# Kernel tuning notes

Hardware: AMD Instinct MI355X
Metric: run time of the kernel (lower is better)

## Reference

```python
import jax, jax.numpy as jnp
import numpy as np

B, L, D, A = 64, 196, 2048, 1024  # batch, locations, hidden_size, att_hid_size


def setup_inputs() -> dict:
    key = jax.random.key(0)
    ks = jax.random.split(key, 8)
    scale = 0.02
    return {
        "att_features": jax.random.normal(ks[0], (B, L, D), dtype=jnp.float32),
        "h": jax.random.normal(ks[1], (B, D), dtype=jnp.float32),
        "W_att": jax.random.normal(ks[2], (D, A), dtype=jnp.float32) * scale,
        "b_att": jnp.zeros((A,), dtype=jnp.float32),
        "W_h": jax.random.normal(ks[3], (D, A), dtype=jnp.float32) * scale,
        "b_h": jnp.zeros((A,), dtype=jnp.float32),
        "w_alpha": jax.random.normal(ks[4], (A, 1), dtype=jnp.float32) * scale,
        "b_alpha": jnp.zeros((1,), dtype=jnp.float32),
    }


def reference(att_features, h, W_att, b_att, W_h, b_h, w_alpha, b_alpha):
    b = att_features.shape[0]
    d = att_features.shape[-1]
    locations = att_features.size // b // d
    af = att_features.reshape(b, locations, d)            # [B, L, D]
    p_att = af @ W_att + b_att                            # [B, L, A]
    p_h = (h @ W_h + b_h)[:, None, :]                     # [B, 1, A]
    scores = (jnp.tanh(p_att + p_h) @ w_alpha + b_alpha)[..., 0]  # [B, L]
    weights = jax.nn.softmax(scores, axis=1)              # [B, L]
    weighted = jnp.einsum('bl,bld->bd', weights, af)      # [B, D]
    return weighted, weights
```

## Files before the change

kernel.cpp:

```cpp
#include <hip/hip_runtime.h>


typedef unsigned short u16;
typedef u16 u16x8 __attribute__((ext_vector_type(8)));
typedef __bf16 bf16x8 __attribute__((ext_vector_type(8)));
typedef float f32x4 __attribute__((ext_vector_type(4)));

#define B_ 64
#define L_ 196
#define D_ 2048
#define A_ 1024
#define M_ (B_ * L_)

__device__ __forceinline__ u16 f2bf(float x) {
  unsigned u = __float_as_uint(x);
  unsigned r = (u + 0x7fffu + ((u >> 16) & 1u)) >> 16;
  return (u16)r;
}

__device__ __forceinline__ float tanh_fast(float x) {
  float e = __expf(2.0f * x);
  return 1.0f - 2.0f / (e + 1.0f);
}

__device__ __forceinline__ void gload_lds16(const void* g, void* l) {
  __builtin_amdgcn_global_load_lds(
      (const __attribute__((address_space(1))) void*)g,
      (__attribute__((address_space(3))) void*)l, 16, 0, 0);
}

__global__ __launch_bounds__(256) void prep_k(
    const float* __restrict__ af, u16* __restrict__ afb,
    const float* __restrict__ W, u16* __restrict__ WT,
    const float* __restrict__ h, const float* __restrict__ Wh,
    float* __restrict__ ph) {
  __shared__ float smem[2112];
  const int bid = blockIdx.x;
  const int t = threadIdx.x;
  if (bid < 256) {
    const int ag = bid & 3, bg = (bid >> 2) & 7, dc = bid >> 5;
    const int d0 = dc * 256;
    for (int i = t; i < 2048; i += 256)
      smem[i] = h[(size_t)(bg * 8 + (i >> 8)) * D_ + d0 + (i & 255)];
    __syncthreads();
    const int a = ag * 256 + t;
    float acc[8] = {};
#pragma unroll 8
    for (int d = 0; d < 256; ++d) {
      float wv = Wh[(size_t)(d0 + d) * A_ + a];
#pragma unroll
      for (int bb = 0; bb < 8; ++bb) acc[bb] += smem[bb * 256 + d] * wv;
    }
#pragma unroll
    for (int bb = 0; bb < 8; ++bb)
      atomicAdd(&ph[(size_t)(bg * 8 + bb) * A_ + a], acc[bb]);
  } else if (bid < 2304) {
    const int tb = bid - 256;
    const int n0 = (tb & 31) * 32, k0 = (tb >> 5) * 32;
    const int tx = t & 31, ty = t >> 5;
    float (*tt)[33] = (float (*)[33])smem;
#pragma unroll
    for (int i = 0; i < 4; ++i)
      tt[ty + i * 8][tx] = W[(size_t)(k0 + ty + i * 8) * A_ + n0 + tx];
    __syncthreads();
#pragma unroll
    for (int i = 0; i < 4; ++i)
      WT[(size_t)(n0 + ty + i * 8) * D_ + k0 + tx] = f2bf(tt[tx][ty + i * 8]);
  } else {
    const int cb = bid - 2304;
    const size_t n = (size_t)M_ * D_;
    for (size_t e = ((size_t)cb * 256 + t) * 8; e < n;
         e += (size_t)2048 * 256 * 8) {
      float4 v0 = *(const float4*)(af + e);
      float4 v1 = *(const float4*)(af + e + 4);
      u16x8 p;
      p[0] = f2bf(v0.x); p[1] = f2bf(v0.y); p[2] = f2bf(v0.z); p[3] = f2bf(v0.w);
      p[4] = f2bf(v1.x); p[5] = f2bf(v1.y); p[6] = f2bf(v1.z); p[7] = f2bf(v1.w);
      *(u16x8*)(afb + e) = p;
    }
  }
}

__global__ __launch_bounds__(512, 2) void gemm8_k(
    const u16* __restrict__ afb, const u16* __restrict__ WT,
    const float* __restrict__ ph, const float* __restrict__ batt,
    const float* __restrict__ bh, const float* __restrict__ walpha,
    float* __restrict__ scores4) {
  __shared__ __align__(16) u16 As[2][2][8192];
  __shared__ __align__(16) u16 Bs[2][2][8192];
  const int tid = threadIdx.x;
  const int lane = tid & 63;
  const int wid = tid >> 6;
  const int wr = wid >> 2;
  const int wc = wid & 3;
  const int wchalf = wc >> 1, wcl = wc & 1;
  const int fr = lane & 15, fq = lane >> 4;

  const int xcd = blockIdx.x & 7, idx = blockIdx.x >> 3;
  const int wg = (xcd < 4 ? xcd * 25 : 100 + (xcd - 4) * 24) + idx;
  const int m0 = (wg >> 2) * 256;
  const int n0 = (wg & 3) * 256;

  int rowc[2], colc[2];
#pragma unroll
  for (int r = 0; r < 2; ++r) {
    int c = r * 512 + tid;
    int s = c >> 6, cw = c & 63;
    rowc[r] = (s >> 1) * 16 + (cw >> 2);
    colc[r] = (s & 1) * 32 + ((((cw & 3) * 16) ^ (((cw >> 5) & 1) * 32)) >> 1);
  }
  const u16* srcA[2][2];
  const u16* srcB[2][2];
#pragma unroll
  for (int hh = 0; hh < 2; ++hh)
#pragma unroll
    for (int r = 0; r < 2; ++r) {
      srcA[hh][r] = afb + (size_t)(m0 + hh * 128 + rowc[r]) * D_ + colc[r];
      srcB[hh][r] = WT + (size_t)(n0 + hh * 128 + rowc[r]) * D_ + colc[r];
    }

  const int laneA = (lane & 15) * 64 + (((lane >> 4) * 16) ^ ((lane & 8) << 2));

  f32x4 acc[8][4] = {};
  u16x8 areg[4][2], breg[4][2];

#define STG_A(BUF, H, KT)                                                    \
  do {                                                                       \
    gload_lds16(srcA[H][0] + (size_t)(KT) * 64, &As[BUF][H][wid * 512]);     \
    gload_lds16(srcA[H][1] + (size_t)(KT) * 64, &As[BUF][H][4096 + wid * 512]); \
  } while (0)
#define STG_B(BUF, H, KT)                                                    \
  do {                                                                       \
    gload_lds16(srcB[H][0] + (size_t)(KT) * 64, &Bs[BUF][H][wid * 512]);     \
    gload_lds16(srcB[H][1] + (size_t)(KT) * 64, &Bs[BUF][H][4096 + wid * 512]); \
  } while (0)
#define LDA_HALF(BF, MH)                                                     \
  do {                                                                       \
    _Pragma("unroll") for (int q = 0; q < 4; ++q) {                          \
      areg[q][0] = *(const u16x8*)&As[BF][wr][((((MH)*4 + q) * 2 + 0) * 1024 + laneA) >> 1]; \
      areg[q][1] = *(const u16x8*)&As[BF][wr][((((MH)*4 + q) * 2 + 1) * 1024 + laneA) >> 1]; \
    }                                                                        \
  } while (0)
#define LDB_PAIR(BF, NQ)                                                     \
  do {                                                                       \
    _Pragma("unroll") for (int nn = 0; nn < 2; ++nn) {                       \
      breg[(NQ)*2 + nn][0] = *(const u16x8*)&Bs[BF][wchalf][(((wcl * 4 + (NQ)*2 + nn) * 2 + 0) * 1024 + laneA) >> 1]; \
      breg[(NQ)*2 + nn][1] = *(const u16x8*)&Bs[BF][wchalf][(((wcl * 4 + (NQ)*2 + nn) * 2 + 1) * 1024 + laneA) >> 1]; \
    }                                                                        \
  } while (0)
#define MM_QUAD(MH, NQ)                                                      \
  do {                                                                       \
    _Pragma("unroll") for (int q = 0; q < 4; ++q)                            \
    _Pragma("unroll") for (int nn = 0; nn < 2; ++nn)                         \
    _Pragma("unroll") for (int kh = 0; kh < 2; ++kh)                         \
      acc[(MH)*4 + q][(NQ)*2 + nn] = __builtin_amdgcn_mfma_f32_16x16x32_bf16( \
          __builtin_bit_cast(bf16x8, areg[q][kh]),                           \
          __builtin_bit_cast(bf16x8, breg[(NQ)*2 + nn][kh]),                 \
          acc[(MH)*4 + q][(NQ)*2 + nn], 0, 0, 0);                            \
  } while (0)
#define PH_PRE()                                                             \
  do {                                                                       \
    __builtin_amdgcn_s_barrier();                                            \
    asm volatile("s_waitcnt lgkmcnt(0)" ::: "memory");                       \
    __builtin_amdgcn_s_setprio(1);                                           \
  } while (0)
#define PH_POST()                                                            \
  do {                                                                       \
    __builtin_amdgcn_s_setprio(0);                                           \
    __builtin_amdgcn_s_barrier();                                            \
  } while (0)
#define KTILE(BF, T, MODE)                                                   \
  do {                                                                       \
    LDA_HALF(BF, 0); LDB_PAIR(BF, 0); LDB_PAIR(BF, 1);                       \
    if ((MODE) <= 1) STG_A((BF) ^ 1, 1, (T) + 1);                            \
    PH_PRE(); MM_QUAD(0, 0); MM_QUAD(0, 1); PH_POST();                       \
    LDA_HALF(BF, 1);                                                         \
    if ((MODE) == 0) { STG_B(BF, 0, (T) + 2); STG_B(BF, 1, (T) + 2);         \
                       STG_A(BF, 0, (T) + 2); }                              \
    PH_PRE(); MM_QUAD(1, 0); MM_QUAD(1, 1);                                  \
    __builtin_amdgcn_s_setprio(0);                                           \
    if ((MODE) == 0) asm volatile("s_waitcnt vmcnt(6)" ::: "memory");        \
    if ((MODE) == 1) asm volatile("s_waitcnt vmcnt(0)" ::: "memory");        \
    if ((MODE) <= 1) __builtin_amdgcn_s_barrier();                           \
  } while (0)

  STG_B(0, 0, 0); STG_B(0, 1, 0); STG_A(0, 0, 0); STG_A(0, 1, 0);
  STG_B(1, 0, 1); STG_B(1, 1, 1); STG_A(1, 0, 1);
  asm volatile("s_waitcnt vmcnt(6)" ::: "memory");
  __builtin_amdgcn_s_barrier();

#pragma unroll 1
  for (int it = 0; it < 15; ++it) {
    const int t = it * 2;
    KTILE(0, t, 0);
    KTILE(1, t + 1, 0);
  }
  KTILE(0, 30, 1);
  KTILE(1, 31, 2);

  const int gnb = n0 + wc * 64 + fr;
  float wa[4], bsv[4], p0[4], p1[4], p2[4];
  const int b0 = m0 / L_;
  const int s1 = (b0 + 1) * L_, s2 = (b0 + 2) * L_;
  const int b1 = (b0 + 1 > 63) ? 63 : b0 + 1;
  const int b2 = (b0 + 2 > 63) ? 63 : b0 + 2;
#pragma unroll
  for (int ni = 0; ni < 4; ++ni) {
    const int gn = gnb + ni * 16;
    wa[ni] = walpha[gn];
    bsv[ni] = batt[gn] + bh[gn];
    p0[ni] = ph[(size_t)b0 * A_ + gn];
    p1[ni] = ph[(size_t)b1 * A_ + gn];
    p2[ni] = ph[(size_t)b2 * A_ + gn];
  }
  float (*redp)[128][4] = (float (*)[128][4])As;
#pragma unroll
  for (int mi = 0; mi < 8; ++mi) {
#pragma unroll
    for (int rr = 0; rr < 4; ++rr) {
      const int lr = mi * 16 + fq * 4 + rr;
      const int gm = m0 + wr * 128 + lr;
      float sp = 0.f;
#pragma unroll
      for (int ni = 0; ni < 4; ++ni) {
        const float pv = (gm >= s2) ? p2[ni] : ((gm >= s1) ? p1[ni] : p0[ni]);
        const float p = acc[mi][ni][rr] + pv + bsv[ni];
        sp += tanh_fast(p) * wa[ni];
      }
      sp += __shfl_xor(sp, 1);
      sp += __shfl_xor(sp, 2);
      sp += __shfl_xor(sp, 4);
      sp += __shfl_xor(sp, 8);
      if (fr == 0) redp[wr][lr][wc] = sp;
    }
  }
  __syncthreads();
  if (tid < 256) {
    f32x4 v = ((const f32x4*)redp)[tid];
    scores4[(size_t)(n0 >> 8) * M_ + m0 + tid] = v[0] + v[1] + v[2] + v[3];
  }
}

__global__ __launch_bounds__(256) void wsum_sm_k(const u16* __restrict__ afb,
                                                 const float* __restrict__ s4,
                                                 float* __restrict__ out) {
  __shared__ float wl[256];
  __shared__ float part[256][8];
  __shared__ float red[4];
  const int b = blockIdx.y;
  const int t = threadIdx.x;

  float s = -1e30f;
  if (t < L_) {
    const int i = b * L_ + t;
    s = s4[i] + s4[M_ + i] + s4[2 * M_ + i] + s4[3 * M_ + i];
  }
  float m = s;
#pragma unroll
  for (int o = 32; o; o >>= 1) m = fmaxf(m, __shfl_xor(m, o));
  if ((t & 63) == 0) red[t >> 6] = m;
  __syncthreads();
  m = fmaxf(fmaxf(red[0], red[1]), fmaxf(red[2], red[3]));
  float e = (t < L_) ? __expf(s - m) : 0.f;
  float sum = e;
#pragma unroll
  for (int o = 32; o; o >>= 1) sum += __shfl_xor(sum, o);
  __syncthreads();
  if ((t & 63) == 0) red[t >> 6] = sum;
  __syncthreads();
  sum = red[0] + red[1] + red[2] + red[3];
  const float w = e / sum;
  wl[t] = w;
  if (t < L_ && blockIdx.x == 0) out[(size_t)B_ * D_ + b * L_ + t] = w;
  __syncthreads();

  const int lq = t >> 6;
  const int dl = t & 63;
  const int d8 = blockIdx.x * 64 + dl;
  float acc[8] = {};
  for (int l = lq * 49; l < lq * 49 + 49; ++l) {
    u16x8 v = *(const u16x8*)(afb + (size_t)(b * L_ + l) * D_ + d8 * 8);
    float ww = wl[l];
#pragma unroll
    for (int j = 0; j < 8; ++j)
      acc[j] += ww * __uint_as_float((unsigned)v[j] << 16);
  }
#pragma unroll
  for (int j = 0; j < 8; ++j) part[t][j] = acc[j];
  __syncthreads();
  if (t < 64) {
    float4 o0, o1;
    o0.x = part[dl][0] + part[64 + dl][0] + part[128 + dl][0] + part[192 + dl][0];
    o0.y = part[dl][1] + part[64 + dl][1] + part[128 + dl][1] + part[192 + dl][1];
    o0.z = part[dl][2] + part[64 + dl][2] + part[128 + dl][2] + part[192 + dl][2];
    o0.w = part[dl][3] + part[64 + dl][3] + part[128 + dl][3] + part[192 + dl][3];
    o1.x = part[dl][4] + part[64 + dl][4] + part[128 + dl][4] + part[192 + dl][4];
    o1.y = part[dl][5] + part[64 + dl][5] + part[128 + dl][5] + part[192 + dl][5];
    o1.z = part[dl][6] + part[64 + dl][6] + part[128 + dl][6] + part[192 + dl][6];
    o1.w = part[dl][7] + part[64 + dl][7] + part[128 + dl][7] + part[192 + dl][7];
    *(float4*)(out + (size_t)b * D_ + d8 * 8) = o0;
    *(float4*)(out + (size_t)b * D_ + d8 * 8 + 4) = o1;
  }
}

extern "C" void kernel_launch(void* const* d_in, const int* in_sizes, int n_in,
                              void* d_out, int out_size, void* d_ws, size_t ws_size,
                              hipStream_t stream) {
  const float* af    = (const float*)d_in[0];
  const float* h     = (const float*)d_in[1];
  const float* W_att = (const float*)d_in[2];
  const float* b_att = (const float*)d_in[3];
  const float* W_h   = (const float*)d_in[4];
  const float* b_h   = (const float*)d_in[5];
  const float* w_al  = (const float*)d_in[6];
  float* out = (float*)d_out;
  char* ws = (char*)d_ws;

  u16* afb       = (u16*)ws;
  u16* WT        = (u16*)(ws + 0x3200000);
  float* ph      = (float*)(ws + 0x3600000);
  float* scores4 = (float*)(ws + 0x3640000);

  hipMemsetAsync(ph, 0, 256u << 10, stream);
  prep_k<<<4352, 256, 0, stream>>>(af, afb, W_att, WT, h, W_h, ph);
  gemm8_k<<<196, 512, 0, stream>>>(afb, WT, ph, b_att, b_h, w_al, scores4);
  wsum_sm_k<<<dim3(4, 64), 256, 0, stream>>>(afb, scores4, out);
}
```

Measured before the change: 119.2 us.

## Load B operand directly from global into registers, dropping LDS staging

The weight (B) tile is no longer staged through shared memory. Each wave loads its own 64 columns straight from global memory into double-buffered registers, while A keeps its LDS double buffer. The hand-tuned pipeline with split phases and explicit vmcnt waits is replaced by a simpler single-barrier-per-tile loop. This halves LDS usage and cuts LDS traffic, but B is now fetched redundantly by the two wave rows, uses more registers, and loses the fine-grained scheduling of the old pipeline.

```diff
diff --git a/kernel.cpp b/kernel.cpp
--- a/kernel.cpp
+++ b/kernel.cpp
@@ -87,13 +87,11 @@
     const float* __restrict__ bh, const float* __restrict__ walpha,
     float* __restrict__ scores4) {
   __shared__ __align__(16) u16 As[2][2][8192];
-  __shared__ __align__(16) u16 Bs[2][2][8192];
   const int tid = threadIdx.x;
   const int lane = tid & 63;
   const int wid = tid >> 6;
   const int wr = wid >> 2;
   const int wc = wid & 3;
-  const int wchalf = wc >> 1, wcl = wc & 1;
   const int fr = lane & 15, fq = lane >> 4;
 
   const int xcd = blockIdx.x & 7, idx = blockIdx.x >> 3;
@@ -110,93 +108,66 @@
     colc[r] = (s & 1) * 32 + ((((cw & 3) * 16) ^ (((cw >> 5) & 1) * 32)) >> 1);
   }
   const u16* srcA[2][2];
-  const u16* srcB[2][2];
 #pragma unroll
   for (int hh = 0; hh < 2; ++hh)
 #pragma unroll
-    for (int r = 0; r < 2; ++r) {
+    for (int r = 0; r < 2; ++r)
       srcA[hh][r] = afb + (size_t)(m0 + hh * 128 + rowc[r]) * D_ + colc[r];
-      srcB[hh][r] = WT + (size_t)(n0 + hh * 128 + rowc[r]) * D_ + colc[r];
-    }
+
+  const u16* bsrc = WT + (size_t)(n0 + wc * 64 + fr) * D_;
 
   const int laneA = (lane & 15) * 64 + (((lane >> 4) * 16) ^ ((lane & 8) << 2));
 
   f32x4 acc[8][4] = {};
-  u16x8 areg[4][2], breg[4][2];
+  u16x8 areg[4];
+  u16x8 bA[4][2], bB[4][2];
 
 #define STG_A(BUF, H, KT)                                                    \
   do {                                                                       \
     gload_lds16(srcA[H][0] + (size_t)(KT) * 64, &As[BUF][H][wid * 512]);     \
     gload_lds16(srcA[H][1] + (size_t)(KT) * 64, &As[BUF][H][4096 + wid * 512]); \
   } while (0)
-#define STG_B(BUF, H, KT)                                                    \
+#define BLOAD(BREG, T)                                                       \
   do {                                                                       \
-    gload_lds16(srcB[H][0] + (size_t)(KT) * 64, &Bs[BUF][H][wid * 512]);     \
-    gload_lds16(srcB[H][1] + (size_t)(KT) * 64, &Bs[BUF][H][4096 + wid * 512]); \
+    _Pragma("unroll") for (int n_ = 0; n_ < 4; ++n_)                         \
+    _Pragma("unroll") for (int kh_ = 0; kh_ < 2; ++kh_)                      \
+      BREG[n_][kh_] = *(const u16x8*)(bsrc + (size_t)n_ * 16 * D_ +          \
+                                      (size_t)(T) * 64 + kh_ * 32 + fq * 8); \
   } while (0)
-#define LDA_HALF(BF, MH)                                                     \
+#define TILE(BF, BCUR, BNXT, T, LAST)                                        \
   do {                                                                       \
-    _Pragma("unroll") for (int q = 0; q < 4; ++q) {                          \
-      areg[q][0] = *(const u16x8*)&As[BF][wr][((((MH)*4 + q) * 2 + 0) * 1024 + laneA) >> 1]; \
-      areg[q][1] = *(const u16x8*)&As[BF][wr][((((MH)*4 + q) * 2 + 1) * 1024 + laneA) >> 1]; \
+    if (!(LAST)) {                                                           \
+      STG_A((BF) ^ 1, 0, (T) + 1);                                           \
+      STG_A((BF) ^ 1, 1, (T) + 1);                                           \
+      BLOAD(BNXT, (T) + 1);                                                  \
     }                                                                        \
+    _Pragma("unroll") for (int mh_ = 0; mh_ < 2; ++mh_)                      \
+    _Pragma("unroll") for (int kh_ = 0; kh_ < 2; ++kh_) {                    \
+      _Pragma("unroll") for (int q_ = 0; q_ < 4; ++q_)                       \
+        areg[q_] = *(const u16x8*)&As[BF][wr][                               \
+            (((mh_ * 4 + q_) * 2 + kh_) * 1024 + laneA) >> 1];               \
+      __builtin_amdgcn_s_setprio(1);                                         \
+      _Pragma("unroll") for (int q_ = 0; q_ < 4; ++q_)                       \
+      _Pragma("unroll") for (int n_ = 0; n_ < 4; ++n_)                       \
+        acc[mh_ * 4 + q_][n_] = __builtin_amdgcn_mfma_f32_16x16x32_bf16(     \
+            __builtin_bit_cast(bf16x8, areg[q_]),                            \
+            __builtin_bit_cast(bf16x8, BCUR[n_][kh_]),                       \
+            acc[mh_ * 4 + q_][n_], 0, 0, 0);                                 \
+      __builtin_amdgcn_s_setprio(0);                                         \
+    }                                                                        \
+    __syncthreads();                                                         \
   } while (0)
-#define LDB_PAIR(BF, NQ)                                                     \
-  do {                                                                       \
-    _Pragma("unroll") for (int nn = 0; nn < 2; ++nn) {                       \
-      breg[(NQ)*2 + nn][0] = *(const u16x8*)&Bs[BF][wchalf][(((wcl * 4 + (NQ)*2 + nn) * 2 + 0) * 1024 + laneA) >> 1]; \
-      breg[(NQ)*2 + nn][1] = *(const u16x8*)&Bs[BF][wchalf][(((wcl * 4 + (NQ)*2 + nn) * 2 + 1) * 1024 + laneA) >> 1]; \
-    }                                                                        \
-  } while (0)
-#define MM_QUAD(MH, NQ)                                                      \
-  do {                                                                       \
-    _Pragma("unroll") for (int q = 0; q < 4; ++q)                            \
-    _Pragma("unroll") for (int nn = 0; nn < 2; ++nn)                         \
-    _Pragma("unroll") for (int kh = 0; kh < 2; ++kh)                         \
-      acc[(MH)*4 + q][(NQ)*2 + nn] = __builtin_amdgcn_mfma_f32_16x16x32_bf16( \
-          __builtin_bit_cast(bf16x8, areg[q][kh]),                           \
-          __builtin_bit_cast(bf16x8, breg[(NQ)*2 + nn][kh]),                 \
-          acc[(MH)*4 + q][(NQ)*2 + nn], 0, 0, 0);                            \
-  } while (0)
-#define PH_PRE()                                                             \
-  do {                                                                       \
-    __builtin_amdgcn_s_barrier();                                            \
-    asm volatile("s_waitcnt lgkmcnt(0)" ::: "memory");                       \
-    __builtin_amdgcn_s_setprio(1);                                           \
-  } while (0)
-#define PH_POST()                                                            \
-  do {                                                                       \
-    __builtin_amdgcn_s_setprio(0);                                           \
-    __builtin_amdgcn_s_barrier();                                            \
-  } while (0)
-#define KTILE(BF, T, MODE)                                                   \
-  do {                                                                       \
-    LDA_HALF(BF, 0); LDB_PAIR(BF, 0); LDB_PAIR(BF, 1);                       \
-    if ((MODE) <= 1) STG_A((BF) ^ 1, 1, (T) + 1);                            \
-    PH_PRE(); MM_QUAD(0, 0); MM_QUAD(0, 1); PH_POST();                       \
-    LDA_HALF(BF, 1);                                                         \
-    if ((MODE) == 0) { STG_B(BF, 0, (T) + 2); STG_B(BF, 1, (T) + 2);         \
-                       STG_A(BF, 0, (T) + 2); }                              \
-    PH_PRE(); MM_QUAD(1, 0); MM_QUAD(1, 1);                                  \
-    __builtin_amdgcn_s_setprio(0);                                           \
-    if ((MODE) == 0) asm volatile("s_waitcnt vmcnt(6)" ::: "memory");        \
-    if ((MODE) == 1) asm volatile("s_waitcnt vmcnt(0)" ::: "memory");        \
-    if ((MODE) <= 1) __builtin_amdgcn_s_barrier();                           \
-  } while (0)
-
-  STG_B(0, 0, 0); STG_B(0, 1, 0); STG_A(0, 0, 0); STG_A(0, 1, 0);
-  STG_B(1, 0, 1); STG_B(1, 1, 1); STG_A(1, 0, 1);
-  asm volatile("s_waitcnt vmcnt(6)" ::: "memory");
-  __builtin_amdgcn_s_barrier();
+
+  STG_A(0, 0, 0);
+  STG_A(0, 1, 0);
+  BLOAD(bA, 0);
+  __syncthreads();
 
 #pragma unroll 1
-  for (int it = 0; it < 15; ++it) {
-    const int t = it * 2;
-    KTILE(0, t, 0);
-    KTILE(1, t + 1, 0);
-  }
-  KTILE(0, 30, 1);
-  KTILE(1, 31, 2);
+  for (int it = 0; it < 16; ++it) {
+    TILE(0, bA, bB, 2 * it, false);
+    TILE(1, bB, bA, 2 * it + 1, (2 * it + 1) == 31);
+  }
 
   const int gnb = n0 + wc * 64 + fr;
   float wa[4], bsv[4], p0[4], p1[4], p2[4];
```

After: 152.0 us. +27.6%, slower.

## Fuse fp32-to-bf16 conversion of activations into GEMM A-tile loading

Applied to the files above, without the earlier changes.

Drops the separate pass that converted the whole activation tensor to bf16 in a workspace. The GEMM now loads fp32 activations into registers, converts them, and writes them into LDS with the swizzled layout. The weighted-sum kernel also reads the fp32 activations directly with twice as many blocks. This removes a full write and re-read of a large bf16 copy, at the cost of reading fp32 (twice the bytes) for A inside the GEMM with register staging instead of direct-to-LDS loads, and a shallower pipeline (prefetch one tile ahead instead of two).

```diff
diff --git a/kernel.cpp b/kernel.cpp
--- a/kernel.cpp
+++ b/kernel.cpp
@@ -30,7 +30,6 @@
 }
 
 __global__ __launch_bounds__(256) void prep_k(
-    const float* __restrict__ af, u16* __restrict__ afb,
     const float* __restrict__ W, u16* __restrict__ WT,
     const float* __restrict__ h, const float* __restrict__ Wh,
     float* __restrict__ ph) {
@@ -54,7 +53,7 @@
 #pragma unroll
     for (int bb = 0; bb < 8; ++bb)
       atomicAdd(&ph[(size_t)(bg * 8 + bb) * A_ + a], acc[bb]);
-  } else if (bid < 2304) {
+  } else {
     const int tb = bid - 256;
     const int n0 = (tb & 31) * 32, k0 = (tb >> 5) * 32;
     const int tx = t & 31, ty = t >> 5;
@@ -66,23 +65,11 @@
 #pragma unroll
     for (int i = 0; i < 4; ++i)
       WT[(size_t)(n0 + ty + i * 8) * D_ + k0 + tx] = f2bf(tt[tx][ty + i * 8]);
-  } else {
-    const int cb = bid - 2304;
-    const size_t n = (size_t)M_ * D_;
-    for (size_t e = ((size_t)cb * 256 + t) * 8; e < n;
-         e += (size_t)2048 * 256 * 8) {
-      float4 v0 = *(const float4*)(af + e);
-      float4 v1 = *(const float4*)(af + e + 4);
-      u16x8 p;
-      p[0] = f2bf(v0.x); p[1] = f2bf(v0.y); p[2] = f2bf(v0.z); p[3] = f2bf(v0.w);
-      p[4] = f2bf(v1.x); p[5] = f2bf(v1.y); p[6] = f2bf(v1.z); p[7] = f2bf(v1.w);
-      *(u16x8*)(afb + e) = p;
-    }
   }
 }
 
 __global__ __launch_bounds__(512, 2) void gemm8_k(
-    const u16* __restrict__ afb, const u16* __restrict__ WT,
+    const float* __restrict__ af, const u16* __restrict__ WT,
     const float* __restrict__ ph, const float* __restrict__ batt,
     const float* __restrict__ bh, const float* __restrict__ walpha,
     float* __restrict__ scores4) {
@@ -101,6 +88,19 @@
   const int m0 = (wg >> 2) * 256;
   const int n0 = (wg & 3) * 256;
 
+  const float* aSrc[4];
+  int aHh[4], aLds[4];
+#pragma unroll
+  for (int r = 0; r < 4; ++r) {
+    const int c = r * 512 + tid;
+    const int hh = c >> 10, cl = c & 1023;
+    const int row = cl >> 3, cc = cl & 7;
+    aHh[r] = hh;
+    aSrc[r] = af + (size_t)(m0 + hh * 128 + row) * D_ + cc * 8;
+    aLds[r] = ((row >> 4) * 2 + (cc >> 2)) * 512 + (row & 15) * 32 +
+              (((cc & 3) * 8) ^ ((row & 8) << 1));
+  }
+
   int rowc[2], colc[2];
 #pragma unroll
   for (int r = 0; r < 2; ++r) {
@@ -109,27 +109,19 @@
     rowc[r] = (s >> 1) * 16 + (cw >> 2);
     colc[r] = (s & 1) * 32 + ((((cw & 3) * 16) ^ (((cw >> 5) & 1) * 32)) >> 1);
   }
-  const u16* srcA[2][2];
   const u16* srcB[2][2];
 #pragma unroll
   for (int hh = 0; hh < 2; ++hh)
 #pragma unroll
-    for (int r = 0; r < 2; ++r) {
-      srcA[hh][r] = afb + (size_t)(m0 + hh * 128 + rowc[r]) * D_ + colc[r];
+    for (int r = 0; r < 2; ++r)
       srcB[hh][r] = WT + (size_t)(n0 + hh * 128 + rowc[r]) * D_ + colc[r];
-    }
 
   const int laneA = (lane & 15) * 64 + (((lane >> 4) * 16) ^ ((lane & 8) << 2));
 
   f32x4 acc[8][4] = {};
   u16x8 areg[4][2], breg[4][2];
 
-#define STG_A(BUF, H, KT)                                                    \
-  do {                                                                       \
-    gload_lds16(srcA[H][0] + (size_t)(KT) * 64, &As[BUF][H][wid * 512]);     \
-    gload_lds16(srcA[H][1] + (size_t)(KT) * 64, &As[BUF][H][4096 + wid * 512]); \
-  } while (0)
-#define STG_B(BUF, H, KT)                                                    \
+#define STG_B2(BUF, H, KT)                                                   \
   do {                                                                       \
     gload_lds16(srcB[H][0] + (size_t)(KT) * 64, &Bs[BUF][H][wid * 512]);     \
     gload_lds16(srcB[H][1] + (size_t)(KT) * 64, &Bs[BUF][H][4096 + wid * 512]); \
@@ -158,45 +150,79 @@
           __builtin_bit_cast(bf16x8, breg[(NQ)*2 + nn][kh]),                 \
           acc[(MH)*4 + q][(NQ)*2 + nn], 0, 0, 0);                            \
   } while (0)
-#define PH_PRE()                                                             \
-  do {                                                                       \
+#define LGKM_BAR()                                                           \
+  do {                                                                       \
+    asm volatile("s_waitcnt lgkmcnt(0)" ::: "memory");                       \
     __builtin_amdgcn_s_barrier();                                            \
-    asm volatile("s_waitcnt lgkmcnt(0)" ::: "memory");                       \
+  } while (0)
+#define TILE(BF, T, MODE)                                                    \
+  do {                                                                       \
+    float4 a4[4][2];                                                         \
+    if ((MODE) == 0) {                                                       \
+      _Pragma("unroll") for (int r = 0; r < 4; ++r) {                        \
+        a4[r][0] = *(const float4*)(aSrc[r] + (size_t)((T) + 1) * 64);       \
+        a4[r][1] = *(const float4*)(aSrc[r] + (size_t)((T) + 1) * 64 + 4);   \
+      }                                                                      \
+      STG_B2((BF) ^ 1, 0, (T) + 1);                                         \
+      STG_B2((BF) ^ 1, 1, (T) + 1);                                         \
+    }                                                                        \
+    LDA_HALF(BF, 0); LDB_PAIR(BF, 0); LDB_PAIR(BF, 1);                       \
+    LGKM_BAR();                                                              \
     __builtin_amdgcn_s_setprio(1);                                           \
-  } while (0)
-#define PH_POST()                                                            \
-  do {                                                                       \
+    MM_QUAD(0, 0); MM_QUAD(0, 1);                                            \
     __builtin_amdgcn_s_setprio(0);                                           \
-    __builtin_amdgcn_s_barrier();                                            \
-  } while (0)
-#define KTILE(BF, T, MODE)                                                   \
-  do {                                                                       \
-    LDA_HALF(BF, 0); LDB_PAIR(BF, 0); LDB_PAIR(BF, 1);                       \
-    if ((MODE) <= 1) STG_A((BF) ^ 1, 1, (T) + 1);                            \
-    PH_PRE(); MM_QUAD(0, 0); MM_QUAD(0, 1); PH_POST();                       \
     LDA_HALF(BF, 1);                                                         \
-    if ((MODE) == 0) { STG_B(BF, 0, (T) + 2); STG_B(BF, 1, (T) + 2);         \
-                       STG_A(BF, 0, (T) + 2); }                              \
-    PH_PRE(); MM_QUAD(1, 0); MM_QUAD(1, 1);                                  \
+    if ((MODE) == 0) {                                                       \
+      _Pragma("unroll") for (int r = 0; r < 4; ++r) {                        \
+        u16x8 p;                                                             \
+        p[0] = f2bf(a4[r][0].x); p[1] = f2bf(a4[r][0].y);                    \
+        p[2] = f2bf(a4[r][0].z); p[3] = f2bf(a4[r][0].w);                    \
+        p[4] = f2bf(a4[r][1].x); p[5] = f2bf(a4[r][1].y);                    \
+        p[6] = f2bf(a4[r][1].z); p[7] = f2bf(a4[r][1].w);                    \
+        *(u16x8*)&As[(BF) ^ 1][aHh[r]][aLds[r]] = p;                         \
+      }                                                                      \
+    }                                                                        \
+    LGKM_BAR();                                                              \
+    __builtin_amdgcn_s_setprio(1);                                           \
+    MM_QUAD(1, 0); MM_QUAD(1, 1);                                            \
     __builtin_amdgcn_s_setprio(0);                                           \
-    if ((MODE) == 0) asm volatile("s_waitcnt vmcnt(6)" ::: "memory");        \
-    if ((MODE) == 1) asm volatile("s_waitcnt vmcnt(0)" ::: "memory");        \
-    if ((MODE) <= 1) __builtin_amdgcn_s_barrier();                           \
-  } while (0)
-
-  STG_B(0, 0, 0); STG_B(0, 1, 0); STG_A(0, 0, 0); STG_A(0, 1, 0);
-  STG_B(1, 0, 1); STG_B(1, 1, 1); STG_A(1, 0, 1);
-  asm volatile("s_waitcnt vmcnt(6)" ::: "memory");
-  __builtin_amdgcn_s_barrier();
+    if ((MODE) == 0) {                                                       \
+      asm volatile("s_waitcnt vmcnt(0)" ::: "memory");                       \
+      LGKM_BAR();                                                            \
+    }                                                                        \
+  } while (0)
+
+  {
+    float4 a4[4][2];
+#pragma unroll
+    for (int r = 0; r < 4; ++r) {
+      a4[r][0] = *(const float4*)(aSrc[r]);
+      a4[r][1] = *(const float4*)(aSrc[r] + 4);
+    }
+    STG_B2(0, 0, 0);
+    STG_B2(0, 1, 0);
+#pragma unroll
+    for (int r = 0; r < 4; ++r) {
+      u16x8 p;
+      p[0] = f2bf(a4[r][0].x); p[1] = f2bf(a4[r][0].y);
+      p[2] = f2bf(a4[r][0].z); p[3] = f2bf(a4[r][0].w);
+      p[4] = f2bf(a4[r][1].x); p[5] = f2bf(a4[r][1].y);
+      p[6] = f2bf(a4[r][1].z); p[7] = f2bf(a4[r][1].w);
+      *(u16x8*)&As[0][aHh[r]][aLds[r]] = p;
+    }
+    asm volatile("s_waitcnt vmcnt(0) lgkmcnt(0)" ::: "memory");
+    __builtin_amdgcn_s_barrier();
+  }
 
 #pragma unroll 1
-  for (int it = 0; it < 15; ++it) {
-    const int t = it * 2;
-    KTILE(0, t, 0);
-    KTILE(1, t + 1, 0);
-  }
-  KTILE(0, 30, 1);
-  KTILE(1, 31, 2);
+  for (int it = 0; it < 16; ++it) {
+    TILE(0, 2 * it, 0);
+    if (it < 15) {
+      TILE(1, 2 * it + 1, 0);
+    } else {
+      TILE(1, 31, 1);
+    }
+  }
 
   const int gnb = n0 + wc * 64 + fr;
   float wa[4], bsv[4], p0[4], p1[4], p2[4];
@@ -213,6 +239,7 @@
     p1[ni] = ph[(size_t)b1 * A_ + gn];
     p2[ni] = ph[(size_t)b2 * A_ + gn];
   }
+  __syncthreads();
   float (*redp)[128][4] = (float (*)[128][4])As;
 #pragma unroll
   for (int mi = 0; mi < 8; ++mi) {
@@ -241,11 +268,11 @@
   }
 }
 
-__global__ __launch_bounds__(256) void wsum_sm_k(const u16* __restrict__ afb,
+__global__ __launch_bounds__(256) void wsum_sm_k(const float* __restrict__ af,
                                                  const float* __restrict__ s4,
                                                  float* __restrict__ out) {
   __shared__ float wl[256];
-  __shared__ float part[256][8];
+  __shared__ f32x4 part[256];
   __shared__ float red[4];
   const int b = blockIdx.y;
   const int t = threadIdx.x;
@@ -276,30 +303,17 @@
 
   const int lq = t >> 6;
   const int dl = t & 63;
-  const int d8 = blockIdx.x * 64 + dl;
-  float acc[8] = {};
+  const int d4 = blockIdx.x * 64 + dl;
+  f32x4 acc = {0.f, 0.f, 0.f, 0.f};
   for (int l = lq * 49; l < lq * 49 + 49; ++l) {
-    u16x8 v = *(const u16x8*)(afb + (size_t)(b * L_ + l) * D_ + d8 * 8);
-    float ww = wl[l];
-#pragma unroll
-    for (int j = 0; j < 8; ++j)
-      acc[j] += ww * __uint_as_float((unsigned)v[j] << 16);
-  }
-#pragma unroll
-  for (int j = 0; j < 8; ++j) part[t][j] = acc[j];
+    f32x4 v = *(const f32x4*)(af + (size_t)(b * L_ + l) * D_ + d4 * 4);
+    acc += v * wl[l];
+  }
+  part[t] = acc;
   __syncthreads();
   if (t < 64) {
-    float4 o0, o1;
-    o0.x = part[dl][0] + part[64 + dl][0] + part[128 + dl][0] + part[192 + dl][0];
-    o0.y = part[dl][1] + part[64 + dl][1] + part[128 + dl][1] + part[192 + dl][1];
-    o0.z = part[dl][2] + part[64 + dl][2] + part[128 + dl][2] + part[192 + dl][2];
-    o0.w = part[dl][3] + part[64 + dl][3] + part[128 + dl][3] + part[192 + dl][3];
-    o1.x = part[dl][4] + part[64 + dl][4] + part[128 + dl][4] + part[192 + dl][4];
-    o1.y = part[dl][5] + part[64 + dl][5] + part[128 + dl][5] + part[192 + dl][5];
-    o1.z = part[dl][6] + part[64 + dl][6] + part[128 + dl][6] + part[192 + dl][6];
-    o1.w = part[dl][7] + part[64 + dl][7] + part[128 + dl][7] + part[192 + dl][7];
-    *(float4*)(out + (size_t)b * D_ + d8 * 8) = o0;
-    *(float4*)(out + (size_t)b * D_ + d8 * 8 + 4) = o1;
+    f32x4 tot = part[t] + part[64 + t] + part[128 + t] + part[192 + t];
+    *(f32x4*)(out + (size_t)b * D_ + d4 * 4) = tot;
   }
 }
 
@@ -316,13 +330,12 @@
   float* out = (float*)d_out;
   char* ws = (char*)d_ws;
 
-  u16* afb       = (u16*)ws;
-  u16* WT        = (u16*)(ws + 0x3200000);
-  float* ph      = (float*)(ws + 0x3600000);
-  float* scores4 = (float*)(ws + 0x3640000);
+  u16* WT        = (u16*)ws;
+  float* ph      = (float*)(ws + 0x400000);
+  float* scores4 = (float*)(ws + 0x440000);
 
   hipMemsetAsync(ph, 0, 256u << 10, stream);
-  prep_k<<<4352, 256, 0, stream>>>(af, afb, W_att, WT, h, W_h, ph);
-  gemm8_k<<<196, 512, 0, stream>>>(afb, WT, ph, b_att, b_h, w_al, scores4);
-  wsum_sm_k<<<dim3(4, 64), 256, 0, stream>>>(afb, scores4, out);
-}
+  prep_k<<<2304, 256, 0, stream>>>(W_att, WT, h, W_h, ph);
+  gemm8_k<<<196, 512, 0, stream>>>(af, WT, ph, b_att, b_h, w_al, scores4);
+  wsum_sm_k<<<dim3(8, 64), 256, 0, stream>>>(af, scores4, out);
+}
```

New measurement: 353.3 us. 2.96x slower.

## Shrink GEMM tile to 256x64 and launch 784 blocks for better CU occupancy

Applied to the files above, without the earlier changes.

Changes the fused GEMM+tanh+score kernel from 256x256 tiles over 196 blocks to 256x64 tiles over 784 blocks. Each wave now owns 32 rows and all 64 columns, so the cross-wave LDS reduction is dropped and every wave writes its partial scores directly. There are now 16 partial score planes, which the softmax kernel sums. The goal is to fill the 256 CUs, since 196 blocks left many idle. The cost is four times more loading of the A operand and lower arithmetic intensity per block.

```diff
diff --git a/kernel.cpp b/kernel.cpp
--- a/kernel.cpp
+++ b/kernel.cpp
@@ -81,25 +81,21 @@
   }
 }
 
-__global__ __launch_bounds__(512, 2) void gemm8_k(
+__global__ __launch_bounds__(512, 4) void gemm8_k(
     const u16* __restrict__ afb, const u16* __restrict__ WT,
     const float* __restrict__ ph, const float* __restrict__ batt,
     const float* __restrict__ bh, const float* __restrict__ walpha,
-    float* __restrict__ scores4) {
+    float* __restrict__ scores16) {
   __shared__ __align__(16) u16 As[2][2][8192];
-  __shared__ __align__(16) u16 Bs[2][2][8192];
+  __shared__ __align__(16) u16 Bs[2][4096];
   const int tid = threadIdx.x;
   const int lane = tid & 63;
   const int wid = tid >> 6;
-  const int wr = wid >> 2;
-  const int wc = wid & 3;
-  const int wchalf = wc >> 1, wcl = wc & 1;
   const int fr = lane & 15, fq = lane >> 4;
 
-  const int xcd = blockIdx.x & 7, idx = blockIdx.x >> 3;
-  const int wg = (xcd < 4 ? xcd * 25 : 100 + (xcd - 4) * 24) + idx;
-  const int m0 = (wg >> 2) * 256;
-  const int n0 = (wg & 3) * 256;
+  const int wg = (blockIdx.x & 7) * 98 + (blockIdx.x >> 3);
+  const int m0 = (wg >> 4) * 256;
+  const int n0 = (wg & 15) * 64;
 
   int rowc[2], colc[2];
 #pragma unroll
@@ -110,53 +106,45 @@
     colc[r] = (s & 1) * 32 + ((((cw & 3) * 16) ^ (((cw >> 5) & 1) * 32)) >> 1);
   }
   const u16* srcA[2][2];
-  const u16* srcB[2][2];
 #pragma unroll
   for (int hh = 0; hh < 2; ++hh)
 #pragma unroll
-    for (int r = 0; r < 2; ++r) {
+    for (int r = 0; r < 2; ++r)
       srcA[hh][r] = afb + (size_t)(m0 + hh * 128 + rowc[r]) * D_ + colc[r];
-      srcB[hh][r] = WT + (size_t)(n0 + hh * 128 + rowc[r]) * D_ + colc[r];
-    }
+  const u16* srcB = WT + (size_t)(n0 + rowc[0]) * D_ + colc[0];
 
   const int laneA = (lane & 15) * 64 + (((lane >> 4) * 16) ^ ((lane & 8) << 2));
-
-  f32x4 acc[8][4] = {};
-  u16x8 areg[4][2], breg[4][2];
+  const int ahh = wid >> 2;
+  const int arow2 = (wid & 3) * 2;
+
+  f32x4 acc[2][4] = {};
+  u16x8 areg[2][2], breg[4][2];
 
 #define STG_A(BUF, H, KT)                                                    \
   do {                                                                       \
     gload_lds16(srcA[H][0] + (size_t)(KT) * 64, &As[BUF][H][wid * 512]);     \
     gload_lds16(srcA[H][1] + (size_t)(KT) * 64, &As[BUF][H][4096 + wid * 512]); \
   } while (0)
-#define STG_B(BUF, H, KT)                                                    \
-  do {                                                                       \
-    gload_lds16(srcB[H][0] + (size_t)(KT) * 64, &Bs[BUF][H][wid * 512]);     \
-    gload_lds16(srcB[H][1] + (size_t)(KT) * 64, &Bs[BUF][H][4096 + wid * 512]); \
-  } while (0)
-#define LDA_HALF(BF, MH)                                                     \
-  do {                                                                       \
-    _Pragma("unroll") for (int q = 0; q < 4; ++q) {                          \
-      areg[q][0] = *(const u16x8*)&As[BF][wr][((((MH)*4 + q) * 2 + 0) * 1024 + laneA) >> 1]; \
-      areg[q][1] = *(const u16x8*)&As[BF][wr][((((MH)*4 + q) * 2 + 1) * 1024 + laneA) >> 1]; \
-    }                                                                        \
-  } while (0)
-#define LDB_PAIR(BF, NQ)                                                     \
-  do {                                                                       \
-    _Pragma("unroll") for (int nn = 0; nn < 2; ++nn) {                       \
-      breg[(NQ)*2 + nn][0] = *(const u16x8*)&Bs[BF][wchalf][(((wcl * 4 + (NQ)*2 + nn) * 2 + 0) * 1024 + laneA) >> 1]; \
-      breg[(NQ)*2 + nn][1] = *(const u16x8*)&Bs[BF][wchalf][(((wcl * 4 + (NQ)*2 + nn) * 2 + 1) * 1024 + laneA) >> 1]; \
-    }                                                                        \
-  } while (0)
-#define MM_QUAD(MH, NQ)                                                      \
-  do {                                                                       \
-    _Pragma("unroll") for (int q = 0; q < 4; ++q)                            \
-    _Pragma("unroll") for (int nn = 0; nn < 2; ++nn)                         \
+#define STG_B(BUF, KT)                                                       \
+  gload_lds16(srcB + (size_t)(KT) * 64, &Bs[BUF][wid * 512])
+#define LDA_MI(BF, MI)                                                       \
+  do {                                                                       \
+    areg[MI][0] = *(const u16x8*)&As[BF][ahh][(((arow2 + (MI)) * 2 + 0) * 1024 + laneA) >> 1]; \
+    areg[MI][1] = *(const u16x8*)&As[BF][ahh][(((arow2 + (MI)) * 2 + 1) * 1024 + laneA) >> 1]; \
+  } while (0)
+#define LDB_ALL(BF)                                                          \
+  do {                                                                       \
+    _Pragma("unroll") for (int ni = 0; ni < 4; ++ni)                         \
     _Pragma("unroll") for (int kh = 0; kh < 2; ++kh)                         \
-      acc[(MH)*4 + q][(NQ)*2 + nn] = __builtin_amdgcn_mfma_f32_16x16x32_bf16( \
-          __builtin_bit_cast(bf16x8, areg[q][kh]),                           \
-          __builtin_bit_cast(bf16x8, breg[(NQ)*2 + nn][kh]),                 \
-          acc[(MH)*4 + q][(NQ)*2 + nn], 0, 0, 0);                            \
+      breg[ni][kh] = *(const u16x8*)&Bs[BF][((ni * 2 + kh) * 1024 + laneA) >> 1]; \
+  } while (0)
+#define MM(MI)                                                               \
+  do {                                                                       \
+    _Pragma("unroll") for (int ni = 0; ni < 4; ++ni)                         \
+    _Pragma("unroll") for (int kh = 0; kh < 2; ++kh)                         \
+      acc[MI][ni] = __builtin_amdgcn_mfma_f32_16x16x32_bf16(                 \
+          __builtin_bit_cast(bf16x8, areg[MI][kh]),                          \
+          __builtin_bit_cast(bf16x8, breg[ni][kh]), acc[MI][ni], 0, 0, 0);   \
   } while (0)
 #define PH_PRE()                                                             \
   do {                                                                       \
@@ -171,34 +159,32 @@
   } while (0)
 #define KTILE(BF, T, MODE)                                                   \
   do {                                                                       \
-    LDA_HALF(BF, 0); LDB_PAIR(BF, 0); LDB_PAIR(BF, 1);                       \
+    LDA_MI(BF, 0); LDB_ALL(BF);                                              \
     if ((MODE) <= 1) STG_A((BF) ^ 1, 1, (T) + 1);                            \
-    PH_PRE(); MM_QUAD(0, 0); MM_QUAD(0, 1); PH_POST();                       \
-    LDA_HALF(BF, 1);                                                         \
-    if ((MODE) == 0) { STG_B(BF, 0, (T) + 2); STG_B(BF, 1, (T) + 2);         \
-                       STG_A(BF, 0, (T) + 2); }                              \
-    PH_PRE(); MM_QUAD(1, 0); MM_QUAD(1, 1);                                  \
+    PH_PRE(); MM(0); PH_POST();                                              \
+    LDA_MI(BF, 1);                                                           \
+    if ((MODE) == 0) { STG_B(BF, (T) + 2); STG_A(BF, 0, (T) + 2); }          \
+    PH_PRE(); MM(1);                                                         \
     __builtin_amdgcn_s_setprio(0);                                           \
-    if ((MODE) == 0) asm volatile("s_waitcnt vmcnt(6)" ::: "memory");        \
+    if ((MODE) == 0) asm volatile("s_waitcnt vmcnt(3)" ::: "memory");        \
     if ((MODE) == 1) asm volatile("s_waitcnt vmcnt(0)" ::: "memory");        \
     if ((MODE) <= 1) __builtin_amdgcn_s_barrier();                           \
   } while (0)
 
-  STG_B(0, 0, 0); STG_B(0, 1, 0); STG_A(0, 0, 0); STG_A(0, 1, 0);
-  STG_B(1, 0, 1); STG_B(1, 1, 1); STG_A(1, 0, 1);
-  asm volatile("s_waitcnt vmcnt(6)" ::: "memory");
+  STG_B(0, 0); STG_A(0, 0, 0); STG_A(0, 1, 0);
+  STG_B(1, 1); STG_A(1, 0, 1);
+  asm volatile("s_waitcnt vmcnt(3)" ::: "memory");
   __builtin_amdgcn_s_barrier();
 
 #pragma unroll 1
   for (int it = 0; it < 15; ++it) {
-    const int t = it * 2;
-    KTILE(0, t, 0);
-    KTILE(1, t + 1, 0);
+    KTILE(0, 2 * it, 0);
+    KTILE(1, 2 * it + 1, 0);
   }
   KTILE(0, 30, 1);
   KTILE(1, 31, 2);
 
-  const int gnb = n0 + wc * 64 + fr;
+  const int gnb = n0 + fr;
   float wa[4], bsv[4], p0[4], p1[4], p2[4];
   const int b0 = m0 / L_;
   const int s1 = (b0 + 1) * L_, s2 = (b0 + 2) * L_;
@@ -213,13 +199,12 @@
     p1[ni] = ph[(size_t)b1 * A_ + gn];
     p2[ni] = ph[(size_t)b2 * A_ + gn];
   }
-  float (*redp)[128][4] = (float (*)[128][4])As;
-#pragma unroll
-  for (int mi = 0; mi < 8; ++mi) {
+  float* sout = scores16 + (size_t)(wg & 15) * M_;
+#pragma unroll
+  for (int mi = 0; mi < 2; ++mi) {
 #pragma unroll
     for (int rr = 0; rr < 4; ++rr) {
-      const int lr = mi * 16 + fq * 4 + rr;
-      const int gm = m0 + wr * 128 + lr;
+      const int gm = m0 + wid * 32 + mi * 16 + fq * 4 + rr;
       float sp = 0.f;
 #pragma unroll
       for (int ni = 0; ni < 4; ++ni) {
@@ -231,18 +216,13 @@
       sp += __shfl_xor(sp, 2);
       sp += __shfl_xor(sp, 4);
       sp += __shfl_xor(sp, 8);
-      if (fr == 0) redp[wr][lr][wc] = sp;
+      if (fr == 0) sout[gm] = sp;
     }
   }
-  __syncthreads();
-  if (tid < 256) {
-    f32x4 v = ((const f32x4*)redp)[tid];
-    scores4[(size_t)(n0 >> 8) * M_ + m0 + tid] = v[0] + v[1] + v[2] + v[3];
-  }
 }
 
 __global__ __launch_bounds__(256) void wsum_sm_k(const u16* __restrict__ afb,
-                                                 const float* __restrict__ s4,
+                                                 const float* __restrict__ s16,
                                                  float* __restrict__ out) {
   __shared__ float wl[256];
   __shared__ float part[256][8];
@@ -253,7 +233,9 @@
   float s = -1e30f;
   if (t < L_) {
     const int i = b * L_ + t;
-    s = s4[i] + s4[M_ + i] + s4[2 * M_ + i] + s4[3 * M_ + i];
+    s = 0.f;
+#pragma unroll
+    for (int g = 0; g < 16; ++g) s += s16[(size_t)g * M_ + i];
   }
   float m = s;
 #pragma unroll
@@ -316,13 +298,13 @@
   float* out = (float*)d_out;
   char* ws = (char*)d_ws;
 
-  u16* afb       = (u16*)ws;
-  u16* WT        = (u16*)(ws + 0x3200000);
-  float* ph      = (float*)(ws + 0x3600000);
-  float* scores4 = (float*)(ws + 0x3640000);
+  u16* afb        = (u16*)ws;
+  u16* WT         = (u16*)(ws + 0x3200000);
+  float* ph       = (float*)(ws + 0x3600000);
+  float* scores16 = (float*)(ws + 0x3640000);
 
   hipMemsetAsync(ph, 0, 256u << 10, stream);
   prep_k<<<4352, 256, 0, stream>>>(af, afb, W_att, WT, h, W_h, ph);
-  gemm8_k<<<196, 512, 0, stream>>>(afb, WT, ph, b_att, b_h, w_al, scores4);
-  wsum_sm_k<<<dim3(4, 64), 256, 0, stream>>>(afb, scores4, out);
-}
+  gemm8_k<<<784, 512, 0, stream>>>(afb, WT, ph, b_att, b_h, w_al, scores16);
+  wsum_sm_k<<<dim3(4, 64), 256, 0, stream>>>(afb, scores16, out);
+}
```

Result: slower. 130.7 us (+9.6%).
